# Kernel tuning notes

Measured on AMD Instinct MI355X. Metric: run time of the kernel, lower is better.

## Reference

```python
import jax, jax.numpy as jnp
import numpy as np

D_MODEL = 1024
H = 16
D_K = D_MODEL // H
NEG = -1e9


def setup_inputs() -> dict:
    key = jax.random.key(0)
    ks = jax.random.split(key, 13)
    B, S = 4, 2048
    q = jax.random.normal(ks[0], (B, S, D_MODEL), dtype=jnp.float32)
    k = jax.random.normal(ks[1], (B, S, D_MODEL), dtype=jnp.float32)
    v = jax.random.normal(ks[2], (B, S, D_MODEL), dtype=jnp.float32)
    mask = jax.random.randint(ks[3], (B, 1, S, S), 0, 2, dtype=jnp.int32)
    s = 1.0 / np.sqrt(D_MODEL)
    wq = jax.random.uniform(ks[4], (D_MODEL, D_MODEL), jnp.float32, -s, s)
    bq = jax.random.uniform(ks[5], (D_MODEL,), jnp.float32, -s, s)
    wk = jax.random.uniform(ks[6], (D_MODEL, D_MODEL), jnp.float32, -s, s)
    bk = jax.random.uniform(ks[7], (D_MODEL,), jnp.float32, -s, s)
    wv = jax.random.uniform(ks[8], (D_MODEL, D_MODEL), jnp.float32, -s, s)
    bv = jax.random.uniform(ks[9], (D_MODEL,), jnp.float32, -s, s)
    wo = jax.random.uniform(ks[10], (D_MODEL, D_MODEL), jnp.float32, -s, s)
    bo = jax.random.uniform(ks[11], (D_MODEL,), jnp.float32, -s, s)
    return {"q": q, "k": k, "v": v, "mask": mask,
            "wq": wq, "bq": bq, "wk": wk, "bk": bk,
            "wv": wv, "bv": bv, "wo": wo, "bo": bo}


def reference(q, k, v, mask, wq, bq, wk, bk, wv, bv, wo, bo):
    B, S, _ = q.shape
    # projections (torch Linear: x @ W.T + b)
    query = q @ wq.T + bq
    key_ = k @ wk.T + bk
    value = v @ wv.T + bv
    # [B, S, H, D_K] -> [B, H, S, D_K]
    query = query.reshape(B, S, H, D_K).transpose(0, 2, 1, 3)
    key_ = key_.reshape(B, S, H, D_K).transpose(0, 2, 1, 3)
    value = value.reshape(B, S, H, D_K).transpose(0, 2, 1, 3)
    scores = jnp.einsum('bhqd,bhkd->bhqk', query, key_) / jnp.sqrt(jnp.float32(D_K))
    scores = jnp.where(mask == 0, jnp.float32(NEG), scores)
    attn = jax.nn.softmax(scores, axis=-1)  # dropout p=0 -> identity
    x = jnp.einsum('bhqk,bhkd->bhqd', attn, value)
    x = x.transpose(0, 2, 1, 3).reshape(B, S, D_MODEL)
    return x @ wo.T + bo
```

## Files before the change

kernel.cpp:

```cpp
#include <hip/hip_runtime.h>
#include <stdint.h>
#include <stddef.h>


typedef unsigned short ushort_t;
typedef unsigned long long u64;
typedef __attribute__((ext_vector_type(8))) short short8;
typedef __attribute__((ext_vector_type(4))) float floatx4;
typedef __attribute__((ext_vector_type(4))) unsigned short ushort4v;
typedef __attribute__((ext_vector_type(4))) unsigned int uint4v;

#define QSCALE (0.125f * 1.4426950408889634f)

__device__ __forceinline__ ushort_t f2bf(float f) {
    union { float ff; unsigned int i; } v; v.ff = f;
    unsigned int u = v.i;
    return (ushort_t)((u + 0x7fffu + ((u >> 16) & 1u)) >> 16);
}
__device__ __forceinline__ unsigned int pack2bf(float a, float b) {
    union { float f; unsigned int i; } ua, ub; ua.f = a; ub.f = b;
    return ((ua.i + 0x8000u) >> 16) | ((ub.i + 0x8000u) & 0xffff0000u);
}
__device__ __forceinline__ float fexp2(float x) {
#if __has_builtin(__builtin_amdgcn_exp2f)
    return __builtin_amdgcn_exp2f(x);
#else
    return exp2f(x);
#endif
}
__device__ __forceinline__ void g2l16(const void* g, void* l) {
    __builtin_amdgcn_global_load_lds(
        (const __attribute__((address_space(1))) void*)(uintptr_t)g,
        (__attribute__((address_space(3))) void*)(uint32_t)(uintptr_t)l,
        16, 0, 0);
}

__global__ __launch_bounds__(256) void conv_w4(
    const float* __restrict__ w0, const float* __restrict__ w1,
    const float* __restrict__ w2, const float* __restrict__ w3,
    ushort_t* __restrict__ out)
{
    const int seg = blockIdx.y;
    const float* src = (seg == 0) ? w0 : (seg == 1) ? w1 : (seg == 2) ? w2 : w3;
    const int i = blockIdx.x * 256 + threadIdx.x;
    const float4 v = ((const float4*)src)[i];
    ushort4v o;
    o.x = f2bf(v.x); o.y = f2bf(v.y); o.z = f2bf(v.z); o.w = f2bf(v.w);
    ((ushort4v*)(out + (size_t)seg * 1024 * 1024))[i] = o;
}

__global__ __launch_bounds__(256) void mask_pack(
    const int* __restrict__ m, u64* __restrict__ out)
{
    const int gid = blockIdx.x * 256 + threadIdx.x;
    const u64 bits = __ballot(m[gid] != 0);
    if ((threadIdx.x & 63) == 0) out[gid >> 6] = bits;
}

template <int MODE, int AF32>
__global__ __launch_bounds__(256, 2) void gemm_bt(
    const void* __restrict__ Ain, const ushort_t* __restrict__ W,
    const float* __restrict__ bias, void* __restrict__ Cout, float scale)
{
    constexpr int N = 1024, K = 1024;
    __shared__ alignas(16) ushort_t As[128 * 32];
    __shared__ alignas(16) ushort_t Bs[128 * 32];

    const int tid  = threadIdx.x;
    const int lane = tid & 63;
    const int w    = tid >> 6;
    const int quad = lane >> 4;
    const int l16  = lane & 15;
    const int wm = w >> 1, wn = w & 1;
    const int bm = blockIdx.x * 128, bn = blockIdx.y * 128;

    const int ar0 = tid >> 2,         acs0 = ((tid & 3) ^ (ar0 & 3)) * 8;
    const int ar1 = (tid + 256) >> 2, acs1 = ((tid & 3) ^ (ar1 & 3)) * 8;

    const ushort_t* Wst0 = W + (size_t)(bn + ar0) * K + acs0;
    const ushort_t* Wst1 = W + (size_t)(bn + ar1) * K + acs1;

    const int arow = tid >> 1, ahalf = tid & 1;
    const float* Af = (const float*)Ain + (size_t)(bm + arow) * K + ahalf * 16;
    const int ac0 = ((2 * ahalf + 0) ^ (arow & 3)) * 8;
    const int ac1 = ((2 * ahalf + 1) ^ (arow & 3)) * 8;

    const ushort_t* Ast0 = (const ushort_t*)Ain + (size_t)(bm + ar0) * K + acs0;
    const ushort_t* Ast1 = (const ushort_t*)Ain + (size_t)(bm + ar1) * K + acs1;

    const int ksw = (quad ^ (l16 & 3)) * 8;
    int asoff[4], bsoff[4];
#pragma unroll
    for (int i = 0; i < 4; i++) {
        asoff[i] = (wm * 64 + i * 16 + l16) * 32 + ksw;
        bsoff[i] = (wn * 64 + i * 16 + l16) * 32 + ksw;
    }

    floatx4 acc[4][4] = {};

    for (int kt = 0; kt < K; kt += 32) {
        float4 f0, f1, f2, f3;
        if (AF32) {
            const float4* ap = (const float4*)(Af + kt);
            f0 = ap[0]; f1 = ap[1]; f2 = ap[2]; f3 = ap[3];
        }
        __syncthreads();
        if (AF32) {
            uint4v c0, c1;
            c0.x = pack2bf(f0.x, f0.y); c0.y = pack2bf(f0.z, f0.w);
            c0.z = pack2bf(f1.x, f1.y); c0.w = pack2bf(f1.z, f1.w);
            c1.x = pack2bf(f2.x, f2.y); c1.y = pack2bf(f2.z, f2.w);
            c1.z = pack2bf(f3.x, f3.y); c1.w = pack2bf(f3.z, f3.w);
            *(uint4v*)&As[arow * 32 + ac0] = c0;
            *(uint4v*)&As[arow * 32 + ac1] = c1;
        } else {
            g2l16(Ast0 + kt, &As[tid * 8]);
            g2l16(Ast1 + kt, &As[(tid + 256) * 8]);
        }
        g2l16(Wst0 + kt, &Bs[tid * 8]);
        g2l16(Wst1 + kt, &Bs[(tid + 256) * 8]);
        __syncthreads();

        short8 af[4], bf[4];
#pragma unroll
        for (int i = 0; i < 4; i++) af[i] = *(const short8*)&As[asoff[i]];
#pragma unroll
        for (int i = 0; i < 4; i++) bf[i] = *(const short8*)&Bs[bsoff[i]];
#pragma unroll
        for (int mi = 0; mi < 4; mi++)
#pragma unroll
            for (int ni = 0; ni < 4; ni++)
                acc[mi][ni] = __builtin_amdgcn_mfma_f32_16x16x32_bf16(
                    af[mi], bf[ni], acc[mi][ni], 0, 0, 0);
    }

#pragma unroll
    for (int ni = 0; ni < 4; ni++) {
        const int n = bn + wn * 64 + ni * 16 + l16;
        const float bv = bias[n];
#pragma unroll
        for (int mi = 0; mi < 4; mi++) {
            const int mbase = bm + wm * 64 + mi * 16 + quad * 4;
            if (MODE == 2) {
                const int b_ = mbase >> 11, s0 = mbase & 2047;
                const int h = n >> 6, d = n & 63;
                ushort4v pk;
#pragma unroll
                for (int r = 0; r < 4; r++)
                    pk[r] = f2bf((acc[mi][ni][r] + bv) * scale);
                *(ushort4v*)&((ushort_t*)Cout)[
                    (((size_t)(b_ * 16 + h)) * 64 + d) * 2048 + s0] = pk;
            } else {
#pragma unroll
                for (int r = 0; r < 4; r++) {
                    const int m = mbase + r;
                    const float of = (acc[mi][ni][r] + bv) * scale;
                    if (MODE == 0) {
                        ((float*)Cout)[(size_t)m * N + n] = of;
                    } else {
                        const int b_ = m >> 11, s = m & 2047;
                        const int h = n >> 6, d = n & 63;
                        ((ushort_t*)Cout)[(((size_t)(b_ * 16 + h)) * 2048 + s) * 64 + d]
                            = f2bf(of);
                    }
                }
            }
        }
    }
}

__global__ __launch_bounds__(256, 3) void attn(
    const ushort_t* __restrict__ Q,
    const ushort_t* __restrict__ Kk,
    const ushort_t* __restrict__ Vt,
    const u64* __restrict__ mb,
    ushort_t* __restrict__ X)
{
    constexpr int S = 2048;
    __shared__ alignas(16) ushort_t Ks[64 * 64];
    __shared__ alignas(16) ushort_t Vs[64 * 64];
    __shared__ alignas(16) ushort_t Ps[4][16 * 64];

    const int tid  = threadIdx.x;
    const int lane = tid & 63;
    const int w    = tid >> 6;
    const int quad = lane >> 4;
    const int l16  = lane & 15;
    const int bh = blockIdx.x;
    const int b  = bh >> 4, h = bh & 15;
    const int qbase = blockIdx.y * 64 + w * 16;
    const int qlane = qbase + l16;

    const int r0 = tid >> 3,         cs0 = ((tid & 7) ^ (r0 & 7)) * 8;
    const int r1 = (tid + 256) >> 3, cs1 = ((tid & 7) ^ (r1 & 7)) * 8;

    const ushort_t* Kst0 = &Kk[((size_t)bh * S + r0) * 64 + cs0];
    const ushort_t* Kst1 = &Kk[((size_t)bh * S + r1) * 64 + cs1];
    const ushort_t* Vst0 = &Vt[((size_t)bh * 64 + r0) * S + cs0];
    const ushort_t* Vst1 = &Vt[((size_t)bh * 64 + r1) * S + cs1];

    const int swz = l16 & 7;
    int kvoff[2][4], pfoff[2], pwoff[4];
#pragma unroll
    for (int ks = 0; ks < 2; ks++) {
        pfoff[ks] = l16 * 64 + (((ks * 4 + quad) ^ swz) * 8);
#pragma unroll
        for (int ni = 0; ni < 4; ni++)
            kvoff[ks][ni] = (ni * 16 + l16) * 64 + (((ks * 4 + quad) ^ swz) * 8);
    }
#pragma unroll
    for (int ni = 0; ni < 4; ni++)
        pwoff[ni] = l16 * 64 + (((ni * 2 + (quad >> 1)) ^ swz) * 8) + (quad & 1) * 4;
    ushort_t* Psw = &Ps[w][0];

    short8 qf[2];
#pragma unroll
    for (int ks = 0; ks < 2; ks++)
        qf[ks] = *(const short8*)&Q[((size_t)bh * S + qlane) * 64 + ks * 32 + quad * 8];

    short8 onesv;
#pragma unroll
    for (int i = 0; i < 8; i++) onesv[i] = (short)0x3F80;

    const u64* mrow = mb + ((size_t)b * S + qlane) * 32;

    floatx4 o[4] = {};
    floatx4 lf = {};

    for (int kt = 0; kt < 32; kt++) {
        __syncthreads();
        g2l16(Kst0 + kt * 4096, &Ks[tid * 8]);
        g2l16(Kst1 + kt * 4096, &Ks[(tid + 256) * 8]);
        g2l16(Vst0 + kt * 64,   &Vs[tid * 8]);
        g2l16(Vst1 + kt * 64,   &Vs[(tid + 256) * 8]);
        __syncthreads();

        floatx4 s[4] = {};
#pragma unroll
        for (int ks = 0; ks < 2; ks++)
#pragma unroll
            for (int ni = 0; ni < 4; ni++)
                s[ni] = __builtin_amdgcn_mfma_f32_16x16x32_bf16(
                    *(const short8*)&Ks[kvoff[ks][ni]], qf[ks], s[ni], 0, 0, 0);

        const u64 mw = mrow[kt];
#pragma unroll
        for (int ni = 0; ni < 4; ni++) {
            const unsigned int t = (unsigned int)(mw >> (ni * 16 + quad * 4));
#pragma unroll
            for (int r = 0; r < 4; r++)
                s[ni][r] = (t & (1u << r)) ? fexp2(s[ni][r]) : 0.f;
        }

#pragma unroll
        for (int ni = 0; ni < 4; ni++) {
            unsigned int lo = pack2bf(s[ni][0], s[ni][1]);
            unsigned int hi = pack2bf(s[ni][2], s[ni][3]);
            unsigned long long dv = ((unsigned long long)hi << 32) | lo;
            *(unsigned long long*)&Psw[pwoff[ni]] = dv;
        }

#pragma unroll
        for (int ks = 0; ks < 2; ks++) {
            const short8 pf = *(const short8*)&Psw[pfoff[ks]];
            lf = __builtin_amdgcn_mfma_f32_16x16x32_bf16(onesv, pf, lf, 0, 0, 0);
#pragma unroll
            for (int ni = 0; ni < 4; ni++)
                o[ni] = __builtin_amdgcn_mfma_f32_16x16x32_bf16(
                    *(const short8*)&Vs[kvoff[ks][ni]], pf, o[ni], 0, 0, 0);
        }
    }

    const float inv = 1.0f / lf[0];
#pragma unroll
    for (int ni = 0; ni < 4; ni++) {
        ushort4v pk;
#pragma unroll
        for (int r = 0; r < 4; r++) pk[r] = f2bf(o[ni][r] * inv);
        *(ushort4v*)&X[((size_t)b * S + qlane) * 1024 + h * 64 + ni * 16 + quad * 4] = pk;
    }
}

extern "C" void kernel_launch(void* const* d_in, const int* in_sizes, int n_in,
                              void* d_out, int out_size, void* d_ws, size_t ws_size,
                              hipStream_t stream) {
    const float* q    = (const float*)d_in[0];
    const float* k    = (const float*)d_in[1];
    const float* v    = (const float*)d_in[2];
    const int*   mask = (const int*)d_in[3];
    const float* wq   = (const float*)d_in[4];
    const float* bq   = (const float*)d_in[5];
    const float* wk   = (const float*)d_in[6];
    const float* bk   = (const float*)d_in[7];
    const float* wv   = (const float*)d_in[8];
    const float* bv   = (const float*)d_in[9];
    const float* wo   = (const float*)d_in[10];
    const float* bo   = (const float*)d_in[11];

    const size_t MB = 1024 * 1024;
    uint8_t* ws = (uint8_t*)d_ws;
    ushort_t* Wb   = (ushort_t*)(ws);
    u64*      mbits= (u64*)(ws + 8 * MB);
    ushort_t* Qp   = (ushort_t*)(ws + 10 * MB);
    ushort_t* Kp   = (ushort_t*)(ws + 26 * MB);
    ushort_t* Vtp  = (ushort_t*)(ws + 42 * MB);
    ushort_t* Xp   = (ushort_t*)(ws + 58 * MB);

    dim3 blk(256);
    dim3 gg(64, 8);
    const int gW = (1024 * 1024) / 1024;
    const int gM = (4 * 2048 * 2048) / 256;

    conv_w4<<<dim3(gW, 4), blk, 0, stream>>>(wq, wk, wv, wo, Wb);
    mask_pack<<<gM, blk, 0, stream>>>(mask, mbits);

    gemm_bt<1, 1><<<gg, blk, 0, stream>>>(q, Wb,                bq, Qp,  QSCALE);
    gemm_bt<1, 1><<<gg, blk, 0, stream>>>(k, Wb + 1 * MB,       bk, Kp,  1.0f);
    gemm_bt<2, 1><<<gg, blk, 0, stream>>>(v, Wb + 2 * MB,       bv, Vtp, 1.0f);

    attn<<<dim3(64, 32), blk, 0, stream>>>(Qp, Kp, Vtp, mbits, Xp);

    gemm_bt<0, 0><<<gg, blk, 0, stream>>>(Xp, Wb + 3 * MB,      bo, d_out, 1.0f);
}
```

Baseline: 475.2 us.

## Double-buffer LDS in GEMM and attention, merge QKV launches, use hardware bf16 pack

Adds double-buffered shared-memory tiles to the projection GEMMs and the attention kernel, so the next K/V or weight tile is fetched while the current one is used, which halves the barriers per iteration. Merges the three QKV projection launches into one grid using a z dimension, and replaces the software bf16 rounding with the v_cvt_pk_bf16_f32 instruction. Raises the attention occupancy hint to 4 blocks per CU. This doubles LDS use, which may limit how many blocks fit per CU, and the runtime mode selection adds a little branching.

Result: faster. 430.8 us (-9.3%).

```diff
diff --git a/kernel.cpp b/kernel.cpp
--- a/kernel.cpp
+++ b/kernel.cpp
@@ -17,9 +17,10 @@
     unsigned int u = v.i;
     return (ushort_t)((u + 0x7fffu + ((u >> 16) & 1u)) >> 16);
 }
-__device__ __forceinline__ unsigned int pack2bf(float a, float b) {
-    union { float f; unsigned int i; } ua, ub; ua.f = a; ub.f = b;
-    return ((ua.i + 0x8000u) >> 16) | ((ub.i + 0x8000u) & 0xffff0000u);
+__device__ __forceinline__ unsigned int pk2(float a, float b) {
+    unsigned int r;
+    asm("v_cvt_pk_bf16_f32 %0, %1, %2" : "=v"(r) : "v"(a), "v"(b));
+    return r;
 }
 __device__ __forceinline__ float fexp2(float x) {
 #if __has_builtin(__builtin_amdgcn_exp2f)
@@ -57,14 +58,15 @@
     if ((threadIdx.x & 63) == 0) out[gid >> 6] = bits;
 }
 
-template <int MODE, int AF32>
-__global__ __launch_bounds__(256, 2) void gemm_bt(
+template <int AF32>
+__device__ __forceinline__ void gemm_core(
     const void* __restrict__ Ain, const ushort_t* __restrict__ W,
-    const float* __restrict__ bias, void* __restrict__ Cout, float scale)
+    const float* __restrict__ bias, void* __restrict__ Cout,
+    float scale, int mode)
 {
     constexpr int N = 1024, K = 1024;
-    __shared__ alignas(16) ushort_t As[128 * 32];
-    __shared__ alignas(16) ushort_t Bs[128 * 32];
+    __shared__ alignas(16) ushort_t As[2][128 * 32];
+    __shared__ alignas(16) ushort_t Bs[2][128 * 32];
 
     const int tid  = threadIdx.x;
     const int lane = tid & 63;
@@ -98,64 +100,87 @@
 
     floatx4 acc[4][4] = {};
 
+    if (AF32) {
+        const float4* ap = (const float4*)Af;
+        const float4 f0 = ap[0], f1 = ap[1], f2 = ap[2], f3 = ap[3];
+        uint4v c0, c1;
+        c0.x = pk2(f0.x, f0.y); c0.y = pk2(f0.z, f0.w);
+        c0.z = pk2(f1.x, f1.y); c0.w = pk2(f1.z, f1.w);
+        c1.x = pk2(f2.x, f2.y); c1.y = pk2(f2.z, f2.w);
+        c1.z = pk2(f3.x, f3.y); c1.w = pk2(f3.z, f3.w);
+        *(uint4v*)&As[0][arow * 32 + ac0] = c0;
+        *(uint4v*)&As[0][arow * 32 + ac1] = c1;
+    } else {
+        g2l16(Ast0, &As[0][tid * 8]);
+        g2l16(Ast1, &As[0][(tid + 256) * 8]);
+    }
+    g2l16(Wst0, &Bs[0][tid * 8]);
+    g2l16(Wst1, &Bs[0][(tid + 256) * 8]);
+    __syncthreads();
+
+    int cur = 0;
     for (int kt = 0; kt < K; kt += 32) {
+        const int nxt = kt + 32;
         float4 f0, f1, f2, f3;
-        if (AF32) {
-            const float4* ap = (const float4*)(Af + kt);
-            f0 = ap[0]; f1 = ap[1]; f2 = ap[2]; f3 = ap[3];
-        }
-        __syncthreads();
-        if (AF32) {
-            uint4v c0, c1;
-            c0.x = pack2bf(f0.x, f0.y); c0.y = pack2bf(f0.z, f0.w);
-            c0.z = pack2bf(f1.x, f1.y); c0.w = pack2bf(f1.z, f1.w);
-            c1.x = pack2bf(f2.x, f2.y); c1.y = pack2bf(f2.z, f2.w);
-            c1.z = pack2bf(f3.x, f3.y); c1.w = pack2bf(f3.z, f3.w);
-            *(uint4v*)&As[arow * 32 + ac0] = c0;
-            *(uint4v*)&As[arow * 32 + ac1] = c1;
-        } else {
-            g2l16(Ast0 + kt, &As[tid * 8]);
-            g2l16(Ast1 + kt, &As[(tid + 256) * 8]);
-        }
-        g2l16(Wst0 + kt, &Bs[tid * 8]);
-        g2l16(Wst1 + kt, &Bs[(tid + 256) * 8]);
-        __syncthreads();
+        if (nxt < K) {
+            if (AF32) {
+                const float4* ap = (const float4*)(Af + nxt);
+                f0 = ap[0]; f1 = ap[1]; f2 = ap[2]; f3 = ap[3];
+            } else {
+                g2l16(Ast0 + nxt, &As[cur ^ 1][tid * 8]);
+                g2l16(Ast1 + nxt, &As[cur ^ 1][(tid + 256) * 8]);
+            }
+            g2l16(Wst0 + nxt, &Bs[cur ^ 1][tid * 8]);
+            g2l16(Wst1 + nxt, &Bs[cur ^ 1][(tid + 256) * 8]);
+        }
 
         short8 af[4], bf[4];
 #pragma unroll
-        for (int i = 0; i < 4; i++) af[i] = *(const short8*)&As[asoff[i]];
-#pragma unroll
-        for (int i = 0; i < 4; i++) bf[i] = *(const short8*)&Bs[bsoff[i]];
+        for (int i = 0; i < 4; i++) af[i] = *(const short8*)&As[cur][asoff[i]];
+#pragma unroll
+        for (int i = 0; i < 4; i++) bf[i] = *(const short8*)&Bs[cur][bsoff[i]];
 #pragma unroll
         for (int mi = 0; mi < 4; mi++)
 #pragma unroll
             for (int ni = 0; ni < 4; ni++)
                 acc[mi][ni] = __builtin_amdgcn_mfma_f32_16x16x32_bf16(
                     af[mi], bf[ni], acc[mi][ni], 0, 0, 0);
+
+        if (AF32 && nxt < K) {
+            uint4v c0, c1;
+            c0.x = pk2(f0.x, f0.y); c0.y = pk2(f0.z, f0.w);
+            c0.z = pk2(f1.x, f1.y); c0.w = pk2(f1.z, f1.w);
+            c1.x = pk2(f2.x, f2.y); c1.y = pk2(f2.z, f2.w);
+            c1.z = pk2(f3.x, f3.y); c1.w = pk2(f3.z, f3.w);
+            *(uint4v*)&As[cur ^ 1][arow * 32 + ac0] = c0;
+            *(uint4v*)&As[cur ^ 1][arow * 32 + ac1] = c1;
+        }
+        __syncthreads();
+        cur ^= 1;
     }
 
 #pragma unroll
     for (int ni = 0; ni < 4; ni++) {
         const int n = bn + wn * 64 + ni * 16 + l16;
-        const float bv = bias[n];
+        const float bv_ = bias[n];
 #pragma unroll
         for (int mi = 0; mi < 4; mi++) {
             const int mbase = bm + wm * 64 + mi * 16 + quad * 4;
-            if (MODE == 2) {
+            if (mode == 2) {
                 const int b_ = mbase >> 11, s0 = mbase & 2047;
                 const int h = n >> 6, d = n & 63;
-                ushort4v pk;
+                ushort4v pk_;
 #pragma unroll
                 for (int r = 0; r < 4; r++)
-                    pk[r] = f2bf((acc[mi][ni][r] + bv) * scale);
+                    pk_[r] = f2bf((acc[mi][ni][r] + bv_) * scale);
                 *(ushort4v*)&((ushort_t*)Cout)[
-                    (((size_t)(b_ * 16 + h)) * 64 + d) * 2048 + s0] = pk;
+                    (((size_t)(b_ * 16 + h)) * 64 + d) * 2048 + s0] = pk_;
             } else {
 #pragma unroll
                 for (int r = 0; r < 4; r++) {
                     const int m = mbase + r;
-                    const float of = (acc[mi][ni][r] + bv) * scale;
-                    if (MODE == 0) {
+                    const float of = (acc[mi][ni][r] + bv_) * scale;
+                    if (mode == 0) {
                         ((float*)Cout)[(size_t)m * N + n] = of;
                     } else {
                         const int b_ = m >> 11, s = m & 2047;
@@ -169,7 +194,32 @@
     }
 }
 
-__global__ __launch_bounds__(256, 3) void attn(
+__global__ __launch_bounds__(256, 2) void gemm_qkv(
+    const float* __restrict__ q, const float* __restrict__ k,
+    const float* __restrict__ v, const ushort_t* __restrict__ Wb,
+    const float* __restrict__ bq, const float* __restrict__ bk,
+    const float* __restrict__ bv,
+    ushort_t* __restrict__ Qp, ushort_t* __restrict__ Kp,
+    ushort_t* __restrict__ Vtp)
+{
+    const int z = blockIdx.z;
+    const float* A = (z == 0) ? q : (z == 1) ? k : v;
+    const ushort_t* W = Wb + (size_t)z * 1024 * 1024;
+    const float* bi = (z == 0) ? bq : (z == 1) ? bk : bv;
+    void* C = (z == 0) ? (void*)Qp : (z == 1) ? (void*)Kp : (void*)Vtp;
+    const float sc = (z == 0) ? QSCALE : 1.0f;
+    const int mode = (z == 2) ? 2 : 1;
+    gemm_core<1>(A, W, bi, C, sc, mode);
+}
+
+__global__ __launch_bounds__(256, 2) void gemm_out(
+    const ushort_t* __restrict__ X, const ushort_t* __restrict__ W,
+    const float* __restrict__ bo, float* __restrict__ out)
+{
+    gemm_core<0>(X, W, bo, out, 1.0f, 0);
+}
+
+__global__ __launch_bounds__(256, 4) void attn(
     const ushort_t* __restrict__ Q,
     const ushort_t* __restrict__ Kk,
     const ushort_t* __restrict__ Vt,
@@ -177,8 +227,8 @@
     ushort_t* __restrict__ X)
 {
     constexpr int S = 2048;
-    __shared__ alignas(16) ushort_t Ks[64 * 64];
-    __shared__ alignas(16) ushort_t Vs[64 * 64];
+    __shared__ alignas(16) ushort_t Ks[2][64 * 64];
+    __shared__ alignas(16) ushort_t Vs[2][64 * 64];
     __shared__ alignas(16) ushort_t Ps[4][16 * 64];
 
     const int tid  = threadIdx.x;
@@ -227,13 +277,22 @@
     floatx4 o[4] = {};
     floatx4 lf = {};
 
+    g2l16(Kst0, &Ks[0][tid * 8]);
+    g2l16(Kst1, &Ks[0][(tid + 256) * 8]);
+    g2l16(Vst0, &Vs[0][tid * 8]);
+    g2l16(Vst1, &Vs[0][(tid + 256) * 8]);
+    __syncthreads();
+
+    int cur = 0;
     for (int kt = 0; kt < 32; kt++) {
-        __syncthreads();
-        g2l16(Kst0 + kt * 4096, &Ks[tid * 8]);
-        g2l16(Kst1 + kt * 4096, &Ks[(tid + 256) * 8]);
-        g2l16(Vst0 + kt * 64,   &Vs[tid * 8]);
-        g2l16(Vst1 + kt * 64,   &Vs[(tid + 256) * 8]);
-        __syncthreads();
+        if (kt < 31) {
+            g2l16(Kst0 + (kt + 1) * 4096, &Ks[cur ^ 1][tid * 8]);
+            g2l16(Kst1 + (kt + 1) * 4096, &Ks[cur ^ 1][(tid + 256) * 8]);
+            g2l16(Vst0 + (kt + 1) * 64,   &Vs[cur ^ 1][tid * 8]);
+            g2l16(Vst1 + (kt + 1) * 64,   &Vs[cur ^ 1][(tid + 256) * 8]);
+        }
+        const ushort_t* Ksc = &Ks[cur][0];
+        const ushort_t* Vsc = &Vs[cur][0];
 
         floatx4 s[4] = {};
 #pragma unroll
@@ -241,7 +300,7 @@
 #pragma unroll
             for (int ni = 0; ni < 4; ni++)
                 s[ni] = __builtin_amdgcn_mfma_f32_16x16x32_bf16(
-                    *(const short8*)&Ks[kvoff[ks][ni]], qf[ks], s[ni], 0, 0, 0);
+                    *(const short8*)&Ksc[kvoff[ks][ni]], qf[ks], s[ni], 0, 0, 0);
 
         const u64 mw = mrow[kt];
 #pragma unroll
@@ -254,9 +313,9 @@
 
 #pragma unroll
         for (int ni = 0; ni < 4; ni++) {
-            unsigned int lo = pack2bf(s[ni][0], s[ni][1]);
-            unsigned int hi = pack2bf(s[ni][2], s[ni][3]);
-            unsigned long long dv = ((unsigned long long)hi << 32) | lo;
+            const unsigned int lo = pk2(s[ni][0], s[ni][1]);
+            const unsigned int hi = pk2(s[ni][2], s[ni][3]);
+            const unsigned long long dv = ((unsigned long long)hi << 32) | lo;
             *(unsigned long long*)&Psw[pwoff[ni]] = dv;
         }
 
@@ -267,17 +326,19 @@
 #pragma unroll
             for (int ni = 0; ni < 4; ni++)
                 o[ni] = __builtin_amdgcn_mfma_f32_16x16x32_bf16(
-                    *(const short8*)&Vs[kvoff[ks][ni]], pf, o[ni], 0, 0, 0);
-        }
+                    *(const short8*)&Vsc[kvoff[ks][ni]], pf, o[ni], 0, 0, 0);
+        }
+        __syncthreads();
+        cur ^= 1;
     }
 
     const float inv = 1.0f / lf[0];
 #pragma unroll
     for (int ni = 0; ni < 4; ni++) {
-        ushort4v pk;
-#pragma unroll
-        for (int r = 0; r < 4; r++) pk[r] = f2bf(o[ni][r] * inv);
-        *(ushort4v*)&X[((size_t)b * S + qlane) * 1024 + h * 64 + ni * 16 + quad * 4] = pk;
+        ushort4v pk_;
+#pragma unroll
+        for (int r = 0; r < 4; r++) pk_[r] = f2bf(o[ni][r] * inv);
+        *(ushort4v*)&X[((size_t)b * S + qlane) * 1024 + h * 64 + ni * 16 + quad * 4] = pk_;
     }
 }
 
@@ -307,18 +368,16 @@
     ushort_t* Xp   = (ushort_t*)(ws + 58 * MB);
 
     dim3 blk(256);
-    dim3 gg(64, 8);
     const int gW = (1024 * 1024) / 1024;
     const int gM = (4 * 2048 * 2048) / 256;
 
     conv_w4<<<dim3(gW, 4), blk, 0, stream>>>(wq, wk, wv, wo, Wb);
     mask_pack<<<gM, blk, 0, stream>>>(mask, mbits);
 
-    gemm_bt<1, 1><<<gg, blk, 0, stream>>>(q, Wb,                bq, Qp,  QSCALE);
-    gemm_bt<1, 1><<<gg, blk, 0, stream>>>(k, Wb + 1 * MB,       bk, Kp,  1.0f);
-    gemm_bt<2, 1><<<gg, blk, 0, stream>>>(v, Wb + 2 * MB,       bv, Vtp, 1.0f);
+    gemm_qkv<<<dim3(64, 8, 3), blk, 0, stream>>>(q, k, v, Wb, bq, bk, bv,
+                                                 Qp, Kp, Vtp);
 
     attn<<<dim3(64, 32), blk, 0, stream>>>(Qp, Kp, Vtp, mbits, Xp);
 
-    gemm_bt<0, 0><<<gg, blk, 0, stream>>>(Xp, Wb + 3 * MB,      bo, d_out, 1.0f);
-}
+    gemm_out<<<dim3(64, 8), blk, 0, stream>>>(Xp, Wb + 3 * MB, bo, (float*)d_out);
+}
```
